# Kernel tuning notes

Measured on AMD Instinct MI355X. Metric: run time of the kernel, lower is better.

Reference implementation:

```python
import jax, jax.numpy as jnp
import numpy as np

B, D, H, W = 8, 128, 152, 272
N_DET = 128
NHEAD = 8
DFF = 512


def _vis_pos_table(d):
    # PositionEmbeddingSine over the fixed 11-entry visibility grid [0,0.1,...,1.0]
    x_embed = jnp.arange(11, dtype=jnp.float32) * 0.1
    dim_t = jnp.arange(d, dtype=jnp.float32)
    dim_t = 10000.0 ** (2.0 * jnp.floor(dim_t / 2.0) / d)
    pos = x_embed[:, None] / dim_t  # [11, d]
    return jnp.stack([jnp.sin(pos[:, 0::2]), jnp.cos(pos[:, 1::2])], axis=2).reshape(11, d)


def _layer_norm(x, g, b, eps=1e-5):
    m = jnp.mean(x, axis=-1, keepdims=True)
    v = jnp.var(x, axis=-1, keepdims=True)
    return (x - m) / jnp.sqrt(v + eps) * g + b


def _adaptive_pool3(x, dets):
    # Faithful AdaptiveAvgPool2d(3) over per-detection crops, vectorized via integral image.
    # x: [B,D,H,W]; dets: [B,N,4] int boxes [x0,y0,x1,y1] with x1>x0, y1>y0.
    P = jnp.cumsum(jnp.cumsum(x, axis=2), axis=3)
    P = jnp.pad(P, ((0, 0), (0, 0), (1, 0), (1, 0)))  # [B,D,H+1,W+1]
    Pt = P.transpose(0, 2, 3, 1)  # [B,H+1,W+1,D]
    sx, sy, ex, ey = dets[..., 0], dets[..., 1], dets[..., 2], dets[..., 3]
    i = jnp.arange(3)

    def edges(s, e):
        # torch adaptive pool bins: start = floor(i*L/3), end = ceil((i+1)*L/3)
        L = (e - s)[..., None]
        st = s[..., None] + (i * L) // 3
        en = s[..., None] + -((-(i + 1) * L) // 3)
        return st, en

    ys, ye = edges(sy, ey)  # [B,N,3]
    xs, xe = edges(sx, ex)
    bidx = jnp.arange(x.shape[0])[:, None, None, None]
    Y0 = ys[:, :, :, None]; Y1 = ye[:, :, :, None]
    X0 = xs[:, :, None, :]; X1 = xe[:, :, None, :]
    g = lambda yy, xx: Pt[bidx, yy, xx]  # [B,N,3,3,D]
    s_ = g(Y1, X1) - g(Y0, X1) - g(Y1, X0) + g(Y0, X0)
    area = ((Y1 - Y0) * (X1 - X0)).astype(x.dtype)  # [B,N,3,3]
    return s_ / area[..., None]  # [B,N,3,3,D] (row-major y,x like .view(128,-1))


def setup_inputs() -> dict:
    key = jax.random.key(0)
    ks = jax.random.split(key, 12)
    x = jax.random.normal(ks[0], (B, D, H, W), jnp.float32)
    vis = jax.random.uniform(ks[1], (B, 1, H, W), jnp.float32)
    # boxes with guaranteed positive extents inside the clamp range (x<=271, y<=151)
    x0 = jax.random.randint(ks[2], (B, N_DET), 0, 230)
    y0 = jax.random.randint(ks[3], (B, N_DET), 0, 110)
    bw = jax.random.randint(ks[4], (B, N_DET), 3, 41)
    bh = jax.random.randint(ks[5], (B, N_DET), 3, 41)
    dets = jnp.stack([x0, y0, x0 + bw, y0 + bh], axis=-1).astype(jnp.int32)
    inds = jax.vmap(lambda k: jax.random.permutation(k, H * W)[:N_DET])(
        jax.random.split(ks[6], B)).astype(jnp.int32)
    s = 1.0 / np.sqrt(D).astype(np.float32)
    Wqkv = jax.random.normal(ks[7], (3 * D, D), jnp.float32) * s
    bqkv = jnp.zeros((3 * D,), jnp.float32)
    Wo = jax.random.normal(ks[8], (D, D), jnp.float32) * s
    bo = jnp.zeros((D,), jnp.float32)
    W1 = jax.random.normal(ks[9], (DFF, D), jnp.float32) * s
    b1 = jnp.zeros((DFF,), jnp.float32)
    W2 = jax.random.normal(ks[10], (D, DFF), jnp.float32) * np.float32(1.0 / np.sqrt(DFF))
    b2 = jnp.zeros((D,), jnp.float32)
    g2 = jnp.ones((D,), jnp.float32); be2 = jnp.zeros((D,), jnp.float32)
    g3 = jnp.ones((D,), jnp.float32); be3 = jnp.zeros((D,), jnp.float32)
    return dict(x=x, vis=vis, dets=dets, inds=inds, Wqkv=Wqkv, bqkv=bqkv, Wo=Wo, bo=bo,
                W1=W1, b1=b1, W2=W2, b2=b2, g2=g2, be2=be2, g3=g3, be3=be3)


def reference(x, vis, dets, inds, Wqkv, bqkv, Wo, bo, W1, b1, W2, b2, g2, be2, g3, be3):
    b, d, h, w = x.shape
    n = inds.shape[1]
    hd = d // NHEAD
    vis_pos = _vis_pos_table(d)  # [11, d]
    # --- query patches: gather point features at detection centers ---
    x_flat = x.transpose(0, 2, 3, 1).reshape(b, h * w, d)
    bidx = jnp.arange(b)[:, None]
    q = x_flat[bidx, inds]  # [b,n,d]
    vis_flat = vis.transpose(0, 2, 3, 1).reshape(b, h * w)
    vidx = (jax.lax.stop_gradient(vis_flat[bidx, inds]) * 10.0).astype(jnp.int32)  # [b,n] in [0,10]
    q = q + vis_pos[vidx]
    # --- key patches: 3x3 adaptive avg pool of each detection crop -> 9 tokens ---
    k = _adaptive_pool3(x, dets).reshape(b * n, 9, d)  # [bn,9,d]
    qf = q.reshape(b * n, 1, d)
    # --- nn.MultiheadAttention cross-attn: batch=b*n detections, L=1 query, S=9 keys ---
    Wq, Wk, Wv = Wqkv[:d], Wqkv[d:2 * d], Wqkv[2 * d:]
    bq, bk, bv = bqkv[:d], bqkv[d:2 * d], bqkv[2 * d:]
    qp = (qf @ Wq.T + bq).reshape(b * n, 1, NHEAD, hd)
    kp = (k @ Wk.T + bk).reshape(b * n, 9, NHEAD, hd)
    vp = (k @ Wv.T + bv).reshape(b * n, 9, NHEAD, hd)
    att = jnp.einsum('blhe,bshe->bhls', qp, kp) / jnp.sqrt(jnp.asarray(hd, x.dtype))
    att = jax.nn.softmax(att, axis=-1)
    ao = jnp.einsum('bhls,bshe->blhe', att, vp).reshape(b * n, 1, d)
    ao = ao @ Wo.T + bo
    # --- post-norm decoder layer (dropout=identity in eval) ---
    t = _layer_norm(qf + ao, g2, be2)
    t2 = jax.nn.relu(t @ W1.T + b1) @ W2.T + b2
    out = _layer_norm(t + t2, g3, be3).reshape(b, n, d)
    # --- scatter refined embeddings back into the feature map ---
    x_flat = x_flat.at[bidx, inds].set(out)
    return x_flat.reshape(b, h, w, d).transpose(0, 3, 1, 2)
```

## Files before the change

kernel.cpp:

```cpp
#include <hip/hip_runtime.h>
#include <math.h>

#define BB 8
#define CH 128
#define HH 152
#define WWID 272
#define HWSZ (HH*WWID)
#define NDET 128
#define NHEAD 8
#define HDIM 16
#define DFF 512
#define NDB (BB*NDET)
#define KSTRIDE 1152
#define CHUNK 16
#define RHALF 76
#define SROW 276

typedef float f4v __attribute__((ext_vector_type(4)));

__device__ __forceinline__ float dot4(float4 w, float4 u, float s) {
    s = fmaf(w.x, u.x, s);
    s = fmaf(w.y, u.y, s);
    s = fmaf(w.z, u.z, s);
    s = fmaf(w.w, u.w, s);
    return s;
}

template<int CTRL, int RMASK>
__device__ __forceinline__ float dpp_add_step(float x) {
    int y = __builtin_amdgcn_update_dpp(0, __builtin_bit_cast(int, x),
                                        CTRL, RMASK, 0xf, false);
    return x + __builtin_bit_cast(float, y);
}
__device__ __forceinline__ float wave_incl_scan(float x) {
    x = dpp_add_step<0x111, 0xf>(x);
    x = dpp_add_step<0x112, 0xf>(x);
    x = dpp_add_step<0x114, 0xf>(x);
    x = dpp_add_step<0x118, 0xf>(x);
    x = dpp_add_step<0x142, 0xa>(x);
    x = dpp_add_step<0x143, 0xc>(x);
    return x;
}

__global__ __launch_bounds__(256) void pool_stream(
    const float* __restrict__ x, const int* __restrict__ dets,
    float* __restrict__ kpart, float* __restrict__ out)
{
    const int bid   = blockIdx.x;
    const int t     = threadIdx.x;
    const int plane = bid >> 1, rhalf = bid & 1;
    const int b     = plane >> 7, ch = plane & 127;
    const int lane  = t & 63,  w  = t >> 6;
    const int rbeg  = rhalf * RHALF;

    __shared__ float S[CHUNK * SROW];

    const float* xp = x + ((size_t)b * CH + ch) * HWSZ;

    {
        const f4v* s4 = (const f4v*)(xp + (size_t)rbeg * WWID);
        f4v* d4 = (f4v*)(out + ((size_t)b * CH + ch) * HWSZ + (size_t)rbeg * WWID);
        #pragma unroll 4
        for (int i = t; i < RHALF * WWID / 4; i += 256) {
            f4v v = s4[i];
            __builtin_nontemporal_store(v, &d4[i]);
        }
    }

    const int d = t & 127, half = t >> 7;
    const int4 dv = *((const int4*)(dets + (size_t)(b * NDET + d) * 4));
    const int sx = dv.x, sy = dv.y, ex = dv.z, ey = dv.w;
    const int Lx = ex - sx, Ly = ey - sy;
    const int xs1 = sx + Lx / 3,        xs2 = sx + 2 * Lx / 3;
    const int xe0 = sx + (Lx + 2) / 3,  xe1 = sx + (2 * Lx + 2) / 3;
    const int ys1 = sy + Ly / 3,        ys2 = sy + 2 * Ly / 3;
    const int ye0 = sy + (Ly + 2) / 3,  ye1 = sy + (2 * Ly + 2) / 3;

    float acc[9] = {0.f,0.f,0.f,0.f,0.f,0.f,0.f,0.f,0.f};

    #pragma unroll 1
    for (int cbeg = rbeg; cbeg < rbeg + RHALF; cbeg += CHUNK) {
        const int csize = (rbeg + RHALF - cbeg < CHUNK) ? (rbeg + RHALF - cbeg) : CHUNK;

        {
            int rl = w;
            f4v vm = (f4v)(0.f), ve = (f4v)(0.f);
            bool have = (rl < csize);
            if (have) {
                const f4v* rowp = (const f4v*)(xp + (size_t)(cbeg + rl) * WWID);
                vm = rowp[lane];
                if (lane < 4) ve = rowp[64 + lane];
            }
            while (have) {
                const int rc = rl;
                f4v v = vm, e = ve;
                rl += 4;
                have = (rl < csize);
                if (have) {
                    const f4v* rowp = (const f4v*)(xp + (size_t)(cbeg + rl) * WWID);
                    vm = rowp[lane];
                    if (lane < 4) ve = rowp[64 + lane];
                }
                float T = v[0] + v[1] + v[2] + v[3];
                float s = wave_incl_scan(T);
                float off0 = s - T;
                float* Sr = S + rc * SROW;
                f4v sm;
                sm[0] = off0;
                sm[1] = off0 + v[0];
                sm[2] = off0 + v[0] + v[1];
                sm[3] = off0 + v[0] + v[1] + v[2];
                *(f4v*)&Sr[4 * lane] = sm;
                float Te = (lane < 4) ? (e[0]+e[1]+e[2]+e[3]) : 0.f;
                float Tei = Te;
                Tei = dpp_add_step<0x111, 0xf>(Tei);
                Tei = dpp_add_step<0x112, 0xf>(Tei);
                float R    = __shfl(s, 63);
                float Esum = __shfl(Tei, 3);
                if (lane < 4) {
                    float offE = R + (Tei - Te);
                    f4v se;
                    se[0] = offE;
                    se[1] = offE + e[0];
                    se[2] = offE + e[0] + e[1];
                    se[3] = offE + e[0] + e[1] + e[2];
                    *(f4v*)&Sr[256 + 4 * lane] = se;
                }
                if (lane == 0) Sr[272] = R + Esum;
            }
        }
        __syncthreads();

        {
            int lo = (sy > cbeg) ? sy : cbeg;
            int hi = (ey < cbeg + csize) ? ey : (cbeg + csize);
            if (lo < hi) {
                int mid = (lo + hi + 1) >> 1;
                int y0 = half ? mid : lo;
                int y1 = half ? hi  : mid;
                for (int y = y0; y < y1; ++y) {
                    const float* Sr = S + (y - cbeg) * SROW;
                    float c0 = Sr[xe0] - Sr[sx];
                    float c1 = Sr[xe1] - Sr[xs1];
                    float c2 = Sr[ex]  - Sr[xs2];
                    float m0 = (y < ye0) ? 1.f : 0.f;
                    float m1 = (y >= ys1 && y < ye1) ? 1.f : 0.f;
                    float m2 = (y >= ys2) ? 1.f : 0.f;
                    acc[0] = fmaf(m0, c0, acc[0]); acc[1] = fmaf(m0, c1, acc[1]); acc[2] = fmaf(m0, c2, acc[2]);
                    acc[3] = fmaf(m1, c0, acc[3]); acc[4] = fmaf(m1, c1, acc[4]); acc[5] = fmaf(m1, c2, acc[5]);
                    acc[6] = fmaf(m2, c0, acc[6]); acc[7] = fmaf(m2, c1, acc[7]); acc[8] = fmaf(m2, c2, acc[8]);
                }
            }
        }
        __syncthreads();
    }

    if (half) {
        #pragma unroll
        for (int j = 0; j < 9; ++j) S[d * 9 + j] = acc[j];
    }
    __syncthreads();
    if (!half) {
        float* kd = kpart + ((size_t)rhalf * NDB + (size_t)(b * NDET + d)) * KSTRIDE + ch;
        #pragma unroll
        for (int j = 0; j < 9; ++j)
            kd[j * CH] = acc[j] + S[d * 9 + j];
    }
}

__global__ __launch_bounds__(256) void tail_kernel(
    const float* __restrict__ x, const float* __restrict__ vis,
    const int* __restrict__ dets, const int* __restrict__ inds,
    const float* __restrict__ kpA, const float* __restrict__ kpB,
    const float* __restrict__ Wqkv, const float* __restrict__ bqkv,
    const float* __restrict__ Wo,   const float* __restrict__ bo,
    const float* __restrict__ W1,   const float* __restrict__ b1,
    const float* __restrict__ W2,   const float* __restrict__ b2,
    const float* __restrict__ g2,   const float* __restrict__ be2,
    const float* __restrict__ g3,   const float* __restrict__ be3,
    float* __restrict__ out)
{
    const int bid = blockIdx.x;
    const int t   = threadIdx.x;
    const int d0  = bid * 2;
    const int b   = d0 >> 7;
    const int o   = t & 127, dl = t >> 7;

    __shared__ float kbuf[2 * 9 * CH];
    __shared__ float kp[2 * 9 * CH];
    __shared__ float vp[2 * 9 * CH];
    __shared__ float invA[2][9];
    __shared__ float qv[2][CH];
    __shared__ float qp[2][CH];
    __shared__ float attl[2][NHEAD][9];
    __shared__ float aov[2][CH];
    __shared__ float Tv[2][CH];
    __shared__ float h1[2][DFF];
    __shared__ float part2[2][2][CH];
    __shared__ float wst[4][2];

    if (t < 18) {
        int dd = t / 9, slot = t - dd * 9;
        const int4 dv = *((const int4*)(dets + (size_t)(b * NDET + ((d0 + dd) & 127)) * 4));
        int sx = dv.x, sy = dv.y, ex = dv.z, ey = dv.w;
        int Lx = ex - sx, Ly = ey - sy;
        int xs1 = sx + Lx / 3,       xs2 = sx + 2 * Lx / 3;
        int xe0 = sx + (Lx + 2) / 3, xe1 = sx + (2 * Lx + 2) / 3;
        int ys1 = sy + Ly / 3,       ys2 = sy + 2 * Ly / 3;
        int ye0 = sy + (Ly + 2) / 3, ye1 = sy + (2 * Ly + 2) / 3;
        int xi = slot % 3, yi = slot / 3;
        int wdt = (xi == 0) ? (xe0 - sx) : (xi == 1) ? (xe1 - xs1) : (ex - xs2);
        int hgt = (yi == 0) ? (ye0 - sy) : (yi == 1) ? (ye1 - ys1) : (ey - ys2);
        invA[dd][slot] = 1.0f / (float)(hgt * wdt);
    }
    {
        int p = inds[b * NDET + ((d0 + dl) & 127)];
        float qval = x[((size_t)b * CH + o) * HWSZ + p];
        float vv   = vis[(size_t)b * HWSZ + p];
        int vidx   = (int)(vv * 10.0f);
        float fr   = powf(10000.0f, -(float)(o & 126) * (1.0f / 128.0f));
        float ang  = 0.1f * (float)vidx * fr;
        qv[dl][o]  = qval + ((o & 1) ? cosf(ang) : sinf(ang));
    }
    __syncthreads();

    for (int i = t; i < 2 * KSTRIDE; i += 256) {
        int dd = (i >= KSTRIDE);
        int r  = i - dd * KSTRIDE;
        int slot = r >> 7;
        float vA = kpA[(size_t)(d0 + dd) * KSTRIDE + r];
        float vB = kpB[(size_t)(d0 + dd) * KSTRIDE + r];
        kbuf[dd * KSTRIDE + r] = (vA + vB) * invA[dd][slot];
    }
    __syncthreads();

    {
        const float4* wr = (const float4*)(Wqkv + (size_t)o * CH);
        const float4* qq = (const float4*)&qv[dl][0];
        float s = 0.f;
        #pragma unroll 8
        for (int i = 0; i < 32; ++i) s = dot4(wr[i], qq[i], s);
        qp[dl][o] = s + bqkv[o];
    }
    {
        const int which = t >> 7;
        const float4* wr = (const float4*)(Wqkv + (size_t)(CH + which * CH + o) * CH);
        float acc[18];
        #pragma unroll
        for (int r = 0; r < 18; ++r) acc[r] = 0.f;
        for (int i = 0; i < 32; ++i) {
            float4 w = wr[i];
            #pragma unroll
            for (int r = 0; r < 18; ++r) {
                float4 a = ((const float4*)kbuf)[r * 32 + i];
                acc[r] = dot4(w, a, acc[r]);
            }
        }
        const float bias = bqkv[CH + which * CH + o];
        float* dst = which ? vp : kp;
        #pragma unroll
        for (int r = 0; r < 18; ++r) dst[r * CH + o] = acc[r] + bias;
    }
    __syncthreads();

    if (o < 72) {
        int h = o / 9, s = o - h * 9;
        const float* qh = &qp[dl][h * HDIM];
        const float* kh = &kp[dl * KSTRIDE + s * CH + h * HDIM];
        float a = 0.f;
        #pragma unroll
        for (int e = 0; e < HDIM; ++e) a = fmaf(qh[e], kh[e], a);
        attl[dl][h][s] = a * 0.25f;
    }
    __syncthreads();
    if (o < 8) {
        float m = attl[dl][o][0];
        #pragma unroll
        for (int s = 1; s < 9; ++s) m = fmaxf(m, attl[dl][o][s]);
        float e[9]; float sum = 0.f;
        #pragma unroll
        for (int s = 0; s < 9; ++s) { e[s] = expf(attl[dl][o][s] - m); sum += e[s]; }
        float inv = 1.0f / sum;
        #pragma unroll
        for (int s = 0; s < 9; ++s) attl[dl][o][s] = e[s] * inv;
    }
    __syncthreads();
    {
        int h = o >> 4;
        float a = 0.f;
        #pragma unroll
        for (int s = 0; s < 9; ++s) a = fmaf(attl[dl][h][s], vp[dl * KSTRIDE + s * CH + o], a);
        aov[dl][o] = a;
    }
    __syncthreads();

    float v1;
    {
        const float4* wr = (const float4*)(Wo + (size_t)o * CH);
        const float4* u4 = (const float4*)&aov[dl][0];
        float s = 0.f;
        #pragma unroll 8
        for (int i = 0; i < 32; ++i) s = dot4(wr[i], u4[i], s);
        v1 = qv[dl][o] + s + bo[o];
    }
    {
        float s1 = v1, s2 = v1 * v1;
        #pragma unroll
        for (int off = 32; off >= 1; off >>= 1) {
            s1 += __shfl_xor(s1, off);
            s2 += __shfl_xor(s2, off);
        }
        if ((t & 63) == 0) { wst[t >> 6][0] = s1; wst[t >> 6][1] = s2; }
    }
    __syncthreads();
    {
        float sum = wst[2 * dl][0] + wst[2 * dl + 1][0];
        float sq  = wst[2 * dl][1] + wst[2 * dl + 1][1];
        float m   = sum * (1.0f / 128.0f);
        float var = sq  * (1.0f / 128.0f) - m * m;
        Tv[dl][o] = (v1 - m) * rsqrtf(var + 1e-5f) * g2[o] + be2[o];
    }
    __syncthreads();

    #pragma unroll
    for (int rep = 0; rep < 2; ++rep) {
        int oo = t + rep * 256;
        const float4* wr = (const float4*)(W1 + (size_t)oo * CH);
        float a0 = 0.f, a1 = 0.f;
        for (int i = 0; i < 32; ++i) {
            float4 w = wr[i];
            a0 = dot4(w, ((const float4*)&Tv[0][0])[i], a0);
            a1 = dot4(w, ((const float4*)&Tv[1][0])[i], a1);
        }
        float bb = b1[oo];
        h1[0][oo] = fmaxf(a0 + bb, 0.f);
        h1[1][oo] = fmaxf(a1 + bb, 0.f);
    }
    __syncthreads();

    {
        const int hf = t >> 7;
        const float4* wr = (const float4*)(W2 + (size_t)o * DFF + hf * (DFF / 2));
        float a0 = 0.f, a1 = 0.f;
        #pragma unroll 4
        for (int i = 0; i < 64; ++i) {
            float4 w = wr[i];
            a0 = dot4(w, ((const float4*)&h1[0][hf * 256])[i], a0);
            a1 = dot4(w, ((const float4*)&h1[1][hf * 256])[i], a1);
        }
        part2[hf][0][o] = a0;
        part2[hf][1][o] = a1;
    }
    __syncthreads();
    float v2 = part2[0][dl][o] + part2[1][dl][o] + b2[o] + Tv[dl][o];
    {
        float s1 = v2, s2 = v2 * v2;
        #pragma unroll
        for (int off = 32; off >= 1; off >>= 1) {
            s1 += __shfl_xor(s1, off);
            s2 += __shfl_xor(s2, off);
        }
        if ((t & 63) == 0) { wst[t >> 6][0] = s1; wst[t >> 6][1] = s2; }
    }
    __syncthreads();
    {
        float sum = wst[2 * dl][0] + wst[2 * dl + 1][0];
        float sq  = wst[2 * dl][1] + wst[2 * dl + 1][1];
        float m   = sum * (1.0f / 128.0f);
        float var = sq  * (1.0f / 128.0f) - m * m;
        float ov  = (v2 - m) * rsqrtf(var + 1e-5f) * g3[o] + be3[o];
        int p = inds[b * NDET + ((d0 + dl) & 127)];
        out[((size_t)b * CH + o) * HWSZ + p] = ov;
    }
}

__global__ __launch_bounds__(256) void copy_x(const f4v* __restrict__ src,
                                              f4v* __restrict__ dst, size_t n4) {
    size_t i = (size_t)blockIdx.x * 256 + threadIdx.x;
    const size_t stride = (size_t)gridDim.x * 256;
    for (; i < n4; i += stride) {
        f4v v = src[i];
        __builtin_nontemporal_store(v, &dst[i]);
    }
}

__device__ __forceinline__ float block_layernorm(float v, int t,
        const float* __restrict__ gamma, const float* __restrict__ beta,
        float* redA, float* redB) {
    float s1 = v, s2 = v * v;
    #pragma unroll
    for (int off = 32; off >= 1; off >>= 1) {
        s1 += __shfl_xor(s1, off);
        s2 += __shfl_xor(s2, off);
    }
    if ((t & 63) == 0) { redA[t >> 6] = s1; redB[t >> 6] = s2; }
    __syncthreads();
    float sum = redA[0] + redA[1] + redA[2] + redA[3];
    float sq  = redB[0] + redB[1] + redB[2] + redB[3];
    __syncthreads();
    float m   = sum * (1.0f / 128.0f);
    float var = sq  * (1.0f / 128.0f) - m * m;
    float r = 0.f;
    if (t < CH) r = (v - m) * rsqrtf(var + 1e-5f) * gamma[t] + beta[t];
    return r;
}

__global__ __launch_bounds__(256) void er_fused_fb(
    const float* __restrict__ x, const float* __restrict__ vis,
    const int* __restrict__ dets, const int* __restrict__ inds,
    const float* __restrict__ Wqkv, const float* __restrict__ bqkv,
    const float* __restrict__ Wo,   const float* __restrict__ bo,
    const float* __restrict__ W1,   const float* __restrict__ b1,
    const float* __restrict__ W2,   const float* __restrict__ b2,
    const float* __restrict__ g2,   const float* __restrict__ be2,
    const float* __restrict__ g3,   const float* __restrict__ be3,
    float* __restrict__ out)
{
    const int bid = blockIdx.x;
    const int t   = threadIdx.x;

    __shared__ float kbuf[9][CH];
    __shared__ float qv[CH];
    __shared__ float qp[CH];
    __shared__ float kp[9][CH];
    __shared__ float vp[9][CH];
    __shared__ float att[NHEAD][9];
    __shared__ float aov[CH];
    __shared__ float tv[CH];
    __shared__ float h1[DFF];
    __shared__ float part[256];
    __shared__ float redA[4], redB[4];
    __shared__ float msk[48][4];

    const int b = bid >> 7;
    const int n = bid & (NDET - 1);

    const int4 dv = *((const int4*)(dets + (size_t)(b * NDET + n) * 4));
    const int sx = dv.x, sy = dv.y, ex = dv.z, ey = dv.w;
    const int Lx = ex - sx, Ly = ey - sy;
    const int xs1 = sx + Lx / 3,        xs2 = sx + 2 * Lx / 3;
    const int xe0 = sx + (Lx + 2) / 3,  xe1 = sx + (2 * Lx + 2) / 3;
    const int ys1 = sy + Ly / 3,        ys2 = sy + 2 * Ly / 3;
    const int ye0 = sy + (Ly + 2) / 3,  ye1 = sy + (2 * Ly + 2) / 3;

    const int p = inds[b * NDET + n];

    if (t < 48) {
        int y = sy + t;
        bool inb = (y < ey);
        msk[t][0] = (inb && y < ye0)              ? 1.f : 0.f;
        msk[t][1] = (inb && y >= ys1 && y < ye1)  ? 1.f : 0.f;
        msk[t][2] = (inb && y >= ys2)             ? 1.f : 0.f;
        msk[t][3] = 0.f;
    }
    if (t < CH) {
        float qval = x[((size_t)b * CH + t) * HWSZ + p];
        float vv   = vis[(size_t)b * HWSZ + p];
        int vidx   = (int)(vv * 10.0f);
        float fr   = powf(10000.0f, -(float)(t & 126) * (1.0f / 128.0f));
        float ang  = 0.1f * (float)vidx * fr;
        float pe   = (t & 1) ? cosf(ang) : sinf(ang);
        qv[t] = qval + pe;
    }
    __syncthreads();

    {
        const int g   = t >> 4;
        const int lx  = t & 15;
        const int sx4 = sx & ~3;
        const int xb  = sx4 + lx * 4;
        const int lxmax = ((ex - 1) - sx4) >> 2;
        const int xba = sx4 + ((lx < lxmax) ? lx : lxmax) * 4;

        float4 mx0, mx1, mx2;
        {
            float m0[4], m1[4], m2[4];
            #pragma unroll
            for (int e = 0; e < 4; ++e) {
                int xx = xb + e;
                m0[e] = (xx >= sx  && xx < xe0) ? 1.f : 0.f;
                m1[e] = (xx >= xs1 && xx < xe1) ? 1.f : 0.f;
                m2[e] = (xx >= xs2 && xx < ex ) ? 1.f : 0.f;
            }
            mx0 = make_float4(m0[0], m0[1], m0[2], m0[3]);
            mx1 = make_float4(m1[0], m1[1], m1[2], m1[3]);
            mx2 = make_float4(m2[0], m2[1], m2[2], m2[3]);
        }

        const int rows_n = ey - sy;
        const int nch    = (rows_n + 7) >> 3;

        for (int c = 0; c < 8; ++c) {
            const int dd = g + c * 16;
            const float* base = x + ((size_t)b * CH + dd) * HWSZ + xba;
            float4 ac0 = make_float4(0.f,0.f,0.f,0.f);
            float4 ac1 = make_float4(0.f,0.f,0.f,0.f);
            float4 ac2 = make_float4(0.f,0.f,0.f,0.f);
            for (int ck = 0; ck < nch; ++ck) {
                const int y0 = sy + (ck << 3);
                float4 v[8];
                #pragma unroll
                for (int k = 0; k < 8; ++k) {
                    int y = y0 + k;
                    y = (y < ey) ? y : (ey - 1);
                    v[k] = *(const float4*)(base + (size_t)y * WWID);
                }
                #pragma unroll
                for (int k = 0; k < 8; ++k) {
                    const float4 m = *(const float4*)&msk[(y0 - sy) + k][0];
                    ac0.x = fmaf(m.x, v[k].x, ac0.x); ac0.y = fmaf(m.x, v[k].y, ac0.y);
                    ac0.z = fmaf(m.x, v[k].z, ac0.z); ac0.w = fmaf(m.x, v[k].w, ac0.w);
                    ac1.x = fmaf(m.y, v[k].x, ac1.x); ac1.y = fmaf(m.y, v[k].y, ac1.y);
                    ac1.z = fmaf(m.y, v[k].z, ac1.z); ac1.w = fmaf(m.y, v[k].w, ac1.w);
                    ac2.x = fmaf(m.z, v[k].x, ac2.x); ac2.y = fmaf(m.z, v[k].y, ac2.y);
                    ac2.z = fmaf(m.z, v[k].z, ac2.z); ac2.w = fmaf(m.z, v[k].w, ac2.w);
                }
            }
            float a[9];
            a[0] = dot4(mx0, ac0, 0.f); a[1] = dot4(mx1, ac0, 0.f); a[2] = dot4(mx2, ac0, 0.f);
            a[3] = dot4(mx0, ac1, 0.f); a[4] = dot4(mx1, ac1, 0.f); a[5] = dot4(mx2, ac1, 0.f);
            a[6] = dot4(mx0, ac2, 0.f); a[7] = dot4(mx1, ac2, 0.f); a[8] = dot4(mx2, ac2, 0.f);
            #pragma unroll
            for (int jj = 0; jj < 9; ++jj) {
                a[jj] += __shfl_xor(a[jj], 8);
                a[jj] += __shfl_xor(a[jj], 4);
                a[jj] += __shfl_xor(a[jj], 2);
                a[jj] += __shfl_xor(a[jj], 1);
            }
            if (lx == 0) {
                int w0 = xe0 - sx, w1 = xe1 - xs1, w2 = ex - xs2;
                int h0 = ye0 - sy, h1r = ye1 - ys1, h2 = ey - ys2;
                kbuf[0][dd] = a[0] / (float)(h0 * w0);
                kbuf[1][dd] = a[1] / (float)(h0 * w1);
                kbuf[2][dd] = a[2] / (float)(h0 * w2);
                kbuf[3][dd] = a[3] / (float)(h1r * w0);
                kbuf[4][dd] = a[4] / (float)(h1r * w1);
                kbuf[5][dd] = a[5] / (float)(h1r * w2);
                kbuf[6][dd] = a[6] / (float)(h2 * w0);
                kbuf[7][dd] = a[7] / (float)(h2 * w1);
                kbuf[8][dd] = a[8] / (float)(h2 * w2);
            }
        }
    }
    __syncthreads();

    if (t < CH) {
        const float4* wr = (const float4*)(Wqkv + (size_t)t * CH);
        const float4* qq = (const float4*)qv;
        float s = 0.f;
        #pragma unroll 8
        for (int i = 0; i < CH / 4; ++i) s = dot4(wr[i], qq[i], s);
        qp[t] = s + bqkv[t];
    }
    {
        const int o = t & (CH - 1);
        const int which = t >> 7;
        const float4* wr = (const float4*)(Wqkv + (size_t)(CH + which * CH + o) * CH);
        float acc[9] = {0.f,0.f,0.f,0.f,0.f,0.f,0.f,0.f,0.f};
        #pragma unroll 4
        for (int i = 0; i < CH / 4; ++i) {
            float4 w = wr[i];
            #pragma unroll
            for (int s = 0; s < 9; ++s) {
                float4 kk = ((const float4*)(&kbuf[s][0]))[i];
                acc[s] = dot4(w, kk, acc[s]);
            }
        }
        float bias = bqkv[CH + which * CH + o];
        if (which == 0) {
            #pragma unroll
            for (int s = 0; s < 9; ++s) kp[s][o] = acc[s] + bias;
        } else {
            #pragma unroll
            for (int s = 0; s < 9; ++s) vp[s][o] = acc[s] + bias;
        }
    }
    __syncthreads();

    if (t < NHEAD * 9) {
        int h = t / 9, s = t - h * 9;
        const float* qh = qp + h * HDIM;
        const float* kh = &kp[s][h * HDIM];
        float a = 0.f;
        #pragma unroll
        for (int e = 0; e < HDIM; ++e) a = fmaf(qh[e], kh[e], a);
        att[h][s] = a * 0.25f;
    }
    __syncthreads();

    if (t < NHEAD) {
        float m = att[t][0];
        #pragma unroll
        for (int s = 1; s < 9; ++s) m = fmaxf(m, att[t][s]);
        float e[9]; float sum = 0.f;
        #pragma unroll
        for (int s = 0; s < 9; ++s) { e[s] = expf(att[t][s] - m); sum += e[s]; }
        float inv = 1.0f / sum;
        #pragma unroll
        for (int s = 0; s < 9; ++s) att[t][s] = e[s] * inv;
    }
    __syncthreads();

    if (t < CH) {
        int h = t >> 4;
        float a = 0.f;
        #pragma unroll
        for (int s = 0; s < 9; ++s) a = fmaf(att[h][s], vp[s][t], a);
        aov[t] = a;
    }
    __syncthreads();

    float v1 = 0.f;
    if (t < CH) {
        const float4* wr = (const float4*)(Wo + (size_t)t * CH);
        const float4* u4 = (const float4*)aov;
        float s = 0.f;
        #pragma unroll 8
        for (int i = 0; i < CH / 4; ++i) s = dot4(wr[i], u4[i], s);
        v1 = qv[t] + s + bo[t];
    }
    float t1 = block_layernorm(v1, t, g2, be2, redA, redB);
    if (t < CH) tv[t] = t1;
    __syncthreads();

    #pragma unroll
    for (int rep = 0; rep < 2; ++rep) {
        int o = t + rep * 256;
        const float4* wr = (const float4*)(W1 + (size_t)o * CH);
        const float4* u4 = (const float4*)tv;
        float s = 0.f;
        #pragma unroll 8
        for (int i = 0; i < CH / 4; ++i) s = dot4(wr[i], u4[i], s);
        h1[o] = fmaxf(s + b1[o], 0.f);
    }
    __syncthreads();

    {
        int o = t & (CH - 1), hf = t >> 7;
        const float4* wr = (const float4*)(W2 + (size_t)o * DFF + hf * (DFF / 2));
        const float4* u4 = (const float4*)(h1 + hf * (DFF / 2));
        float s = 0.f;
        #pragma unroll 8
        for (int i = 0; i < DFF / 8; ++i) s = dot4(wr[i], u4[i], s);
        part[t] = s;
    }
    __syncthreads();

    float v2 = 0.f;
    if (t < CH) {
        float t2 = part[t] + part[t + 128] + b2[t];
        v2 = tv[t] + t2;
    }
    float outv = block_layernorm(v2, t, g3, be3, redA, redB);
    if (t < CH) out[((size_t)b * CH + t) * HWSZ + p] = outv;
}

extern "C" void kernel_launch(void* const* d_in, const int* in_sizes, int n_in,
                              void* d_out, int out_size, void* d_ws, size_t ws_size,
                              hipStream_t stream) {
    const float* x    = (const float*)d_in[0];
    const float* vis  = (const float*)d_in[1];
    const int*   dets = (const int*)d_in[2];
    const int*   inds = (const int*)d_in[3];
    const float* Wqkv = (const float*)d_in[4];
    const float* bqkv = (const float*)d_in[5];
    const float* Wo   = (const float*)d_in[6];
    const float* bo   = (const float*)d_in[7];
    const float* W1   = (const float*)d_in[8];
    const float* b1   = (const float*)d_in[9];
    const float* W2   = (const float*)d_in[10];
    const float* b2   = (const float*)d_in[11];
    const float* g2   = (const float*)d_in[12];
    const float* be2  = (const float*)d_in[13];
    const float* g3   = (const float*)d_in[14];
    const float* be3  = (const float*)d_in[15];
    float* out = (float*)d_out;

    const size_t SZ_KP = (size_t)NDB * KSTRIDE;
    const size_t need  = 2 * SZ_KP * sizeof(float);

    const size_t N4 = (size_t)BB * CH * HWSZ / 4;
    if (ws_size >= need) {
        float* kpA = (float*)d_ws;
        float* kpB = kpA + SZ_KP;

        pool_stream<<<dim3(2048), dim3(256), 0, stream>>>(x, dets, kpA, out);
        tail_kernel<<<dim3(512), dim3(256), 0, stream>>>(
            x, vis, dets, inds, kpA, kpB, Wqkv, bqkv, Wo, bo,
            W1, b1, W2, b2, g2, be2, g3, be3, out);
    } else {
        copy_x<<<dim3(2048), dim3(256), 0, stream>>>(
            (const f4v*)x, (f4v*)out, N4);
        er_fused_fb<<<dim3(NDB), dim3(256), 0, stream>>>(
            x, vis, dets, inds, Wqkv, bqkv, Wo, bo, W1, b1, W2, b2,
            g2, be2, g3, be3, out);
    }
}
```

Before: 173.1 us.

## Move feature-map copy from pool kernel into tail kernel, scatter rows separately

The full x-to-out copy is taken out of the pooling kernel and done by extra blocks appended to the tail kernel grid, so the copy runs alongside the per-detection transformer work. Tail results are staged in a workspace row buffer, and a new small kernel scatters them into the output afterwards so the copy cannot overwrite them. This costs an extra launch and a re-read of x, which the pool kernel has already streamed once, and it needs more workspace.

New measurement: 152.0 us. -12.2%, faster.

```diff
diff --git a/kernel.cpp b/kernel.cpp
--- a/kernel.cpp
+++ b/kernel.cpp
@@ -15,6 +15,8 @@
 #define CHUNK 16
 #define RHALF 76
 #define SROW 276
+#define NTAIL 512
+#define NCOPY 2048
 
 typedef float f4v __attribute__((ext_vector_type(4)));
 
@@ -42,9 +44,9 @@
     return x;
 }
 
-__global__ __launch_bounds__(256) void pool_stream(
+__global__ __launch_bounds__(256) void pool_only(
     const float* __restrict__ x, const int* __restrict__ dets,
-    float* __restrict__ kpart, float* __restrict__ out)
+    float* __restrict__ kpart)
 {
     const int bid   = blockIdx.x;
     const int t     = threadIdx.x;
@@ -56,16 +58,6 @@
     __shared__ float S[CHUNK * SROW];
 
     const float* xp = x + ((size_t)b * CH + ch) * HWSZ;
-
-    {
-        const f4v* s4 = (const f4v*)(xp + (size_t)rbeg * WWID);
-        f4v* d4 = (f4v*)(out + ((size_t)b * CH + ch) * HWSZ + (size_t)rbeg * WWID);
-        #pragma unroll 4
-        for (int i = t; i < RHALF * WWID / 4; i += 256) {
-            f4v v = s4[i];
-            __builtin_nontemporal_store(v, &d4[i]);
-        }
-    }
 
     const int d = t & 127, half = t >> 7;
     const int4 dv = *((const int4*)(dets + (size_t)(b * NDET + d) * 4));
@@ -168,7 +160,7 @@
     }
 }
 
-__global__ __launch_bounds__(256) void tail_kernel(
+__global__ __launch_bounds__(256) void tail_copy(
     const float* __restrict__ x, const float* __restrict__ vis,
     const int* __restrict__ dets, const int* __restrict__ inds,
     const float* __restrict__ kpA, const float* __restrict__ kpB,
@@ -178,10 +170,24 @@
     const float* __restrict__ W2,   const float* __restrict__ b2,
     const float* __restrict__ g2,   const float* __restrict__ be2,
     const float* __restrict__ g3,   const float* __restrict__ be3,
-    float* __restrict__ out)
+    float* __restrict__ rowsb, float* __restrict__ out)
 {
     const int bid = blockIdx.x;
     const int t   = threadIdx.x;
+
+    if (bid >= NTAIL) {
+        const size_t n4 = (size_t)BB * CH * HWSZ / 4;
+        const f4v* s4 = (const f4v*)x;
+        f4v* o4 = (f4v*)out;
+        size_t i = (size_t)(bid - NTAIL) * 256 + t;
+        const size_t stride = (size_t)NCOPY * 256;
+        for (; i < n4; i += stride) {
+            f4v v = s4[i];
+            __builtin_nontemporal_store(v, &o4[i]);
+        }
+        return;
+    }
+
     const int d0  = bid * 2;
     const int b   = d0 >> 7;
     const int o   = t & 127, dl = t >> 7;
@@ -369,9 +375,19 @@
         float m   = sum * (1.0f / 128.0f);
         float var = sq  * (1.0f / 128.0f) - m * m;
         float ov  = (v2 - m) * rsqrtf(var + 1e-5f) * g3[o] + be3[o];
-        int p = inds[b * NDET + ((d0 + dl) & 127)];
-        out[((size_t)b * CH + o) * HWSZ + p] = ov;
-    }
+        rowsb[(size_t)(d0 + dl) * CH + o] = ov;
+    }
+}
+
+__global__ __launch_bounds__(256) void scatter_rows(const float* __restrict__ rows,
+                                                    const int* __restrict__ inds,
+                                                    float* __restrict__ out) {
+    int i = blockIdx.x * 256 + threadIdx.x;
+    int dd = i & (CH - 1);
+    int bn = i >> 7;
+    int b  = bn >> 7;
+    int p  = inds[bn];
+    out[((size_t)b * CH + dd) * HWSZ + p] = rows[i];
 }
 
 __global__ __launch_bounds__(256) void copy_x(const f4v* __restrict__ src,
@@ -676,18 +692,22 @@
     const float* be3  = (const float*)d_in[15];
     float* out = (float*)d_out;
 
-    const size_t SZ_KP = (size_t)NDB * KSTRIDE;
-    const size_t need  = 2 * SZ_KP * sizeof(float);
+    const size_t SZ_KP   = (size_t)NDB * KSTRIDE;
+    const size_t SZ_ROWS = (size_t)NDB * CH;
+    const size_t need = (2 * SZ_KP + SZ_ROWS) * sizeof(float);
 
     const size_t N4 = (size_t)BB * CH * HWSZ / 4;
     if (ws_size >= need) {
-        float* kpA = (float*)d_ws;
-        float* kpB = kpA + SZ_KP;
-
-        pool_stream<<<dim3(2048), dim3(256), 0, stream>>>(x, dets, kpA, out);
-        tail_kernel<<<dim3(512), dim3(256), 0, stream>>>(
+        float* kpA  = (float*)d_ws;
+        float* kpB  = kpA + SZ_KP;
+        float* rows = kpB + SZ_KP;
+
+        pool_only<<<dim3(2048), dim3(256), 0, stream>>>(x, dets, kpA);
+        tail_copy<<<dim3(NTAIL + NCOPY), dim3(256), 0, stream>>>(
             x, vis, dets, inds, kpA, kpB, Wqkv, bqkv, Wo, bo,
-            W1, b1, W2, b2, g2, be2, g3, be3, out);
+            W1, b1, W2, b2, g2, be2, g3, be3, rows, out);
+        scatter_rows<<<dim3((NDB * CH) / 256), dim3(256), 0, stream>>>(
+            rows, inds, out);
     } else {
         copy_x<<<dim3(2048), dim3(256), 0, stream>>>(
             (const f4v*)x, (f4v*)out, N4);
```
